# Performance work log

Measured on AMD Instinct MI355X. Metric: run time of the kernel, lower is better.

The kernel has to match this reference:

```python
import jax, jax.numpy as jnp
import numpy as np

T, B, D, H, DH = 2048, 2, 1024, 16, 64


def _rel_shift(x):
    # x: (Q, R, B, H) -- standard Transformer-XL relative shift via pad/reshape
    Q, R = x.shape[0], x.shape[1]
    zero_pad = jnp.zeros((Q, 1) + x.shape[2:], dtype=x.dtype)
    xp = jnp.concatenate([zero_pad, x], axis=1)          # (Q, R+1, B, H)
    xp = xp.reshape((R + 1, Q) + x.shape[2:])            # (R+1, Q, B, H)
    return xp[1:].reshape(x.shape)                       # (Q, R, B, H)


def setup_inputs() -> dict:
    key = jax.random.key(0)
    ks = jax.random.split(key, 7)
    w = jax.random.normal(ks[0], (T, B, D), dtype=jnp.float32)
    r = jax.random.normal(ks[1], (T, D), dtype=jnp.float32)
    w_qkv = jax.random.normal(ks[2], (3 * H * DH, D), dtype=jnp.float32) * 0.02
    w_r = jax.random.normal(ks[3], (H * DH, D), dtype=jnp.float32) * 0.02
    w_o = jax.random.normal(ks[4], (D, H * DH), dtype=jnp.float32) * 0.02
    r_r_bias = jax.random.normal(ks[5], (H, DH), dtype=jnp.float32) * 0.02
    attn_mask = jax.random.uniform(ks[6], (T, B)) < 0.1
    return {"w": w, "r": r, "w_qkv": w_qkv, "w_r": w_r, "w_o": w_o,
            "r_r_bias": r_r_bias, "attn_mask": attn_mask}


def reference(w, r, w_qkv, w_r, w_o, r_r_bias, attn_mask):
    qlen, bsz, d_model = w.shape
    n_head, d_head = r_r_bias.shape
    rlen = r.shape[0]
    scale = 1.0 / d_head ** 0.5

    heads = jnp.einsum('tbd,ed->tbe', w, w_qkv)           # (T, B, 3*H*DH)
    q, k, v = jnp.split(heads, 3, axis=-1)
    q = q.reshape(qlen, bsz, n_head, d_head)
    k = k.reshape(qlen, bsz, n_head, d_head)
    v = v.reshape(qlen, bsz, n_head, d_head)
    r_head_k = jnp.einsum('rd,ed->re', r, w_r).reshape(rlen, n_head, d_head)

    # NOTE: source uses r_r_bias for BOTH content and position biases
    rq = q + r_r_bias[None, None]                         # (Q, B, H, DH)
    AC = jnp.einsum('qbhd,kbhd->bhqk', rq, k)             # content scores
    BD = jnp.einsum('qbhd,rhd->bhqr', rq, r_head_k)       # position scores

    BD = jnp.transpose(BD, (2, 3, 0, 1))                  # (Q, R, B, H)
    BD = _rel_shift(BD)
    BD = jnp.transpose(BD, (2, 3, 0, 1))                  # (B, H, Q, R)
    BD = BD[:, :, :, :qlen]                               # klen == qlen

    score = (AC + BD) * scale                             # (B, H, Q, K)
    # key-padding mask (K, B) -> broadcast (B, 1, 1, K)
    score = jnp.where(attn_mask.T[:, None, None, :], -jnp.inf, score)

    prob = jax.nn.softmax(score.astype(jnp.float32), axis=-1).astype(score.dtype)
    attn_vec = jnp.einsum('bhqk,kbhd->qbhd', prob, v).reshape(qlen, bsz, n_head * d_head)
    out = jnp.einsum('qbe,de->qbd', attn_vec, w_o)        # (Q, B, D)
    return out, prob
```

## Files before the change

kernel.cpp:

```cpp
#include <hip/hip_runtime.h>
#include <hip/hip_bf16.h>
#include <cstdint>
#include <cstddef>

#define TLEN 2048
#define NB 2
#define DMODEL 1024
#define NH 16
#define NDH 64

typedef unsigned short ushortT;
typedef short bf16x8 __attribute__((ext_vector_type(8)));
typedef float f32x16 __attribute__((ext_vector_type(16)));

__device__ __forceinline__ ushortT f2bf(float f) {
  union { float f; unsigned int u; } x{f};
  unsigned int r = x.u + 0x7fff + ((x.u >> 16) & 1);
  return (ushortT)(r >> 16);
}
__device__ __forceinline__ unsigned int pk2(float lo, float hi) {
  return ((unsigned int)f2bf(hi) << 16) | (unsigned int)f2bf(lo);
}
__device__ __forceinline__ float bf2f(ushortT u) {
  union { unsigned int u; float f; } x;
  x.u = ((unsigned int)u) << 16;
  return x.f;
}

__device__ __forceinline__ void gld_lds16(const void* g, void* l) {
  __builtin_amdgcn_global_load_lds(
      (const __attribute__((address_space(1))) unsigned int*)g,
      (__attribute__((address_space(3))) unsigned int*)l, 16, 0, 0);
}


__global__ __launch_bounds__(256) void cvt_bf16(const float* __restrict__ in,
                                                ushortT* __restrict__ out, int n4) {
  int i = blockIdx.x * 256 + threadIdx.x;
  if (i < n4) {
    float4 v = reinterpret_cast<const float4*>(in)[i];
    ushort4 o;
    o.x = f2bf(v.x); o.y = f2bf(v.y); o.z = f2bf(v.z); o.w = f2bf(v.w);
    reinterpret_cast<ushort4*>(out)[i] = o;
  }
}

__global__ __launch_bounds__(256) void cvt_mask(const int* __restrict__ mask,
                                                float* __restrict__ mfl) {
  int j = blockIdx.x * 256 + threadIdx.x;
  if (j < TLEN) {
    mfl[j]        = mask[j * NB]     ? 0.f : 1.f;
    mfl[TLEN + j] = mask[j * NB + 1] ? 0.f : 1.f;
  }
}


template <typename Epi>
__global__ __launch_bounds__(256) void gemm_bf16(const ushortT* __restrict__ A,
                                                 const ushortT* __restrict__ B,
                                                 int K, Epi epi) {
  __shared__ ushortT Al[128 * 64];
  __shared__ ushortT Bl[128 * 64];
  const int tid = threadIdx.x;
  const int lane = tid & 63;
  const int wv = tid >> 6;
  const int wm = wv >> 1, wn = wv & 1;
  const int m0 = blockIdx.y * 128;
  const int n0 = blockIdx.x * 128;
  const int r32 = lane & 31;
  const int hh = lane >> 5;

  f32x16 acc[2][2];
#pragma unroll
  for (int i = 0; i < 2; ++i)
#pragma unroll
    for (int j = 0; j < 2; ++j)
#pragma unroll
      for (int e = 0; e < 16; ++e) acc[i][j][e] = 0.f;

  for (int k0 = 0; k0 < K; k0 += 64) {
#pragma unroll
    for (int it = 0; it < 4; ++it) {
      int idx = it * 256 + tid;
      int r = idx >> 3, c = idx & 7;
      int gcol = k0 + ((c ^ (r & 7)) << 3);
      gld_lds16(A + (size_t)(m0 + r) * K + gcol, Al + idx * 8);
      gld_lds16(B + (size_t)(n0 + r) * K + gcol, Bl + idx * 8);
    }
    asm volatile("s_waitcnt vmcnt(0)");
    __syncthreads();
#pragma unroll
    for (int kc = 0; kc < 4; ++kc) {
      int lc = kc * 2 + hh;
      bf16x8 af[2], bfr[2];
#pragma unroll
      for (int f = 0; f < 2; ++f) {
        int ar = wm * 64 + f * 32 + r32;
        af[f] = *(const bf16x8*)(Al + ar * 64 + ((lc ^ (ar & 7)) << 3));
        int br = wn * 64 + f * 32 + r32;
        bfr[f] = *(const bf16x8*)(Bl + br * 64 + ((lc ^ (br & 7)) << 3));
      }
#pragma unroll
      for (int i = 0; i < 2; ++i)
#pragma unroll
        for (int j = 0; j < 2; ++j)
          acc[i][j] = __builtin_amdgcn_mfma_f32_32x32x16_bf16(af[i], bfr[j],
                                                              acc[i][j], 0, 0, 0);
    }
    __syncthreads();
  }

#pragma unroll
  for (int i = 0; i < 2; ++i)
#pragma unroll
    for (int j = 0; j < 2; ++j)
#pragma unroll
      for (int rg = 0; rg < 16; ++rg) {
        int m = m0 + wm * 64 + i * 32 + (rg & 3) + 8 * (rg >> 2) + 4 * hh;
        int n = n0 + wn * 64 + j * 32 + r32;
        epi.store(m, n, acc[i][j][rg]);
      }
}

struct EpiQKV {
  ushortT* qb; ushortT* kb; ushortT* vtb; const float* bias;
  __device__ void store(int m, int n, float val) const {
    int t = m >> 1, b = m & 1;
    int which = n >> 10;
    int h = (n >> 6) & (NH - 1);
    int dh = n & (NDH - 1);
    int bh = b * NH + h;
    if (which == 0)
      qb[((size_t)bh * TLEN + t) * NDH + dh] = f2bf(val + bias[(h << 6) | dh]);
    else if (which == 1)
      kb[((size_t)bh * TLEN + t) * NDH + dh] = f2bf(val);
    else
      vtb[((size_t)bh * NDH + dh) * TLEN + t] = f2bf(val);
  }
};

struct EpiRK {
  ushortT* rk;
  __device__ void store(int m, int n, float val) const {
    int h = n >> 6, dh = n & 63;
    rk[((size_t)h * TLEN + m) * NDH + dh] = f2bf(val);
  }
};

struct EpiOut {
  float* out;
  __device__ void store(int m, int n, float val) const {
    out[(size_t)m * DMODEL + n] = val;
  }
};


__global__ __launch_bounds__(256) void attn_fast(
    const ushortT* __restrict__ qb, const ushortT* __restrict__ kb,
    const ushortT* __restrict__ vtb, const ushortT* __restrict__ rkb,
    const float* __restrict__ mfl, unsigned int* __restrict__ S,
    float* __restrict__ linv_g, ushortT* __restrict__ av_bf) {
  __shared__ float W[4][64][32];
  __shared__ float sl[4][32];

  const int bh = blockIdx.y;
  const int b = bh >> 4, h = bh & 15;
  const int wv = threadIdx.x >> 6;
  const int lane = threadIdx.x & 63;
  const int ql = lane & 31;
  const int hh = lane >> 5;
  const int qtile = wv & 1;
  const int jh = wv >> 1;
  const int q0 = blockIdx.x * 64 + qtile * 32;
  const int qg = q0 + ql;

  const ushortT* Qbh = qb + (size_t)bh * TLEN * NDH;
  const ushortT* Kbh = kb + (size_t)bh * TLEN * NDH;
  const ushortT* Vbh = vtb + (size_t)bh * NDH * TLEN;
  const ushortT* Rh  = rkb + (size_t)h * TLEN * NDH;
  const float* mflb  = mfl + (size_t)b * TLEN;
  unsigned int* Sb   = S + (size_t)bh * (TLEN / 2) * TLEN;
  float (*Wp)[32] = W[wv];

  bf16x8 Qf[4], Qs[4];
  {
    int r2 = min(qg + 1, TLEN - 1);
#pragma unroll
    for (int c = 0; c < 4; ++c) {
      Qf[c] = *(const bf16x8*)(Qbh + (size_t)qg * NDH + c * 16 + hh * 8);
      Qs[c] = *(const bf16x8*)(Qbh + (size_t)r2 * NDH + c * 16 + hh * 8);
    }
  }

  f32x16 pacc0, pacc1;
#pragma unroll
  for (int i = 0; i < 16; ++i) { pacc0[i] = 0.f; pacc1[i] = 0.f; }
  float l_acc = 0.f;

  const int jbeg = jh * (TLEN / 2);
  const int jend = jbeg + (TLEN / 2);
  for (int j0 = jbeg; j0 < jend; j0 += 32) {
    const int w1b = 2016 - q0 + j0;
    const int w2b = j0 - q0 - 33;
    const int base0 = (j0 <= q0) ? w1b : w2b;
    const int base1 = ((j0 < q0) ? w1b : w2b) + 32;
    const bool t0w1 = (j0 <= q0);
    const bool t1w1 = (j0 < q0);

    int r0 = max(0, min(base0 + ql, TLEN - 1));
    int r1 = max(0, min(base1 + ql, TLEN - 1));
    const ushortT* s0 = Rh + (size_t)r0 * NDH + hh * 8;
    const ushortT* s1 = Rh + (size_t)r1 * NDH + hh * 8;
    const ushortT* sk = Kbh + (size_t)(j0 + ql) * NDH + hh * 8;
    const ushortT* vrow0 = Vbh + (size_t)ql * TLEN + j0 + 8 * hh;
    const ushortT* vrow1 = Vbh + (size_t)(32 + ql) * TLEN + j0 + 8 * hh;
    bf16x8 rk0[4], rk1[4], kk[4];
#pragma unroll
    for (int c = 0; c < 4; ++c) {
      rk0[c] = *(const bf16x8*)(s0 + c * 16);
      rk1[c] = *(const bf16x8*)(s1 + c * 16);
      kk[c]  = *(const bf16x8*)(sk + c * 16);
    }
    bf16x8 v00 = *(const bf16x8*)(vrow0);
    bf16x8 v01 = *(const bf16x8*)(vrow0 + 16);
    bf16x8 v10 = *(const bf16x8*)(vrow1);
    bf16x8 v11 = *(const bf16x8*)(vrow1 + 16);
    float4 mf4[4];
#pragma unroll
    for (int g = 0; g < 4; ++g)
      mf4[g] = *(const float4*)(mflb + j0 + 8 * g + 4 * hh);

    f32x16 facc;
#pragma unroll
    for (int i = 0; i < 16; ++i) facc[i] = 0.f;
    __builtin_amdgcn_s_setprio(1);
#pragma unroll
    for (int c = 0; c < 4; ++c)
      facc = __builtin_amdgcn_mfma_f32_32x32x16_bf16(rk0[c], t0w1 ? Qf[c] : Qs[c], facc, 0, 0, 0);
    __builtin_amdgcn_s_setprio(0);
#pragma unroll
    for (int r = 0; r < 16; ++r)
      Wp[(r & 3) + 8 * (r >> 2) + 4 * hh][ql] = facc[r];

#pragma unroll
    for (int i = 0; i < 16; ++i) facc[i] = 0.f;
    __builtin_amdgcn_s_setprio(1);
#pragma unroll
    for (int c = 0; c < 4; ++c)
      facc = __builtin_amdgcn_mfma_f32_32x32x16_bf16(rk1[c], t1w1 ? Qf[c] : Qs[c], facc, 0, 0, 0);
    __builtin_amdgcn_s_setprio(0);
#pragma unroll
    for (int r = 0; r < 16; ++r)
      Wp[32 + (r & 3) + 8 * (r >> 2) + 4 * hh][ql] = facc[r];

    f32x16 cacc;
#pragma unroll
    for (int i = 0; i < 16; ++i) cacc[i] = 0.f;
    __builtin_amdgcn_s_setprio(1);
#pragma unroll
    for (int c = 0; c < 4; ++c)
      cacc = __builtin_amdgcn_mfma_f32_32x32x16_bf16(kk[c], Qf[c], cacc, 0, 0, 0);
    __builtin_amdgcn_s_setprio(0);

    float p[16];
#pragma unroll
    for (int r = 0; r < 16; ++r) {
      int jrow = (r & 3) + 8 * (r >> 2) + 4 * hh;
      int jg = j0 + jrow;
      float bd = (jg == qg + 1) ? 0.f : Wp[jrow - ql + 31][ql];
      float sc = (cacc[r] + bd) * 0.125f;
      float mv = (&mf4[r >> 2].x)[r & 3];
      float pv = mv * __expf(sc);
      p[r] = pv;
      l_acc += pv;
    }

    unsigned int u[8];
#pragma unroll
    for (int i = 0; i < 8; ++i) u[i] = pk2(p[2 * i], p[2 * i + 1]);

#pragma unroll
    for (int i = 0; i < 8; ++i) {
      int r = 2 * i;
      int jrow = (r & 3) + 8 * (r >> 2) + 4 * hh;
      Sb[(size_t)((j0 + jrow) >> 1) * TLEN + qg] = u[i];
    }

#pragma unroll
    for (int kh = 0; kh < 2; ++kh) {
      unsigned int t0 = (unsigned int)__shfl_xor((int)u[4 * kh + 0], 32);
      unsigned int t1 = (unsigned int)__shfl_xor((int)u[4 * kh + 1], 32);
      unsigned int t2 = (unsigned int)__shfl_xor((int)u[4 * kh + 2], 32);
      unsigned int t3 = (unsigned int)__shfl_xor((int)u[4 * kh + 3], 32);
      unsigned int fr[4];
      fr[0] = hh ? t2 : u[4 * kh + 0];
      fr[1] = hh ? t3 : u[4 * kh + 1];
      fr[2] = hh ? u[4 * kh + 2] : t0;
      fr[3] = hh ? u[4 * kh + 3] : t1;
      bf16x8 pa = *reinterpret_cast<bf16x8*>(fr);
      __builtin_amdgcn_s_setprio(1);
      pacc0 = __builtin_amdgcn_mfma_f32_32x32x16_bf16(pa, kh ? v01 : v00, pacc0, 0, 0, 0);
      pacc1 = __builtin_amdgcn_mfma_f32_32x32x16_bf16(pa, kh ? v11 : v10, pacc1, 0, 0, 0);
      __builtin_amdgcn_s_setprio(0);
    }
  }

#pragma unroll
  for (int r = 0; r < 16; ++r) {
    int qrow = (r & 3) + 8 * (r >> 2) + 4 * hh;
    Wp[qrow][ql] = pacc0[r];
    Wp[32 + qrow][ql] = pacc1[r];
  }
  float lh = l_acc + __shfl_xor(l_acc, 32);
  if (lane < 32) sl[wv][ql] = lh;
  __syncthreads();

  if (wv < 2) {
    if (lane < 32) {
      float lt = sl[wv][ql] + sl[wv + 2][ql];
      linv_g[(size_t)bh * TLEN + q0 + ql] = 1.0f / lt;
    }
#pragma unroll
    for (int r = 0; r < 16; ++r) {
      int qrow = (r & 3) + 8 * (r >> 2) + 4 * hh;
      float lt = sl[wv][qrow] + sl[wv + 2][qrow];
      float iv = 1.0f / lt;
      float s0v = W[wv][qrow][ql] + W[wv + 2][qrow][ql];
      float s1v = W[wv][32 + qrow][ql] + W[wv + 2][32 + qrow][ql];
      size_t aoff = ((size_t)(q0 + qrow) * NB + b) * DMODEL + h * NDH;
      av_bf[aoff + ql] = f2bf(s0v * iv);
      av_bf[aoff + 32 + ql] = f2bf(s1v * iv);
    }
  }
}


__global__ __launch_bounds__(256) void rescale_t(const unsigned int* __restrict__ S,
                                                 const float* __restrict__ linv_g,
                                                 float* __restrict__ prob) {
  __shared__ unsigned int lds[64][65];
  __shared__ float liv[64];
  const int qt = blockIdx.x;
  const int jt = blockIdx.y;
  const int bh = blockIdx.z;
  const int t = threadIdx.x;

  const unsigned int* Sb = S + ((size_t)bh * (TLEN / 2) + jt * 64) * TLEN + qt * 64;
  {
    int row = t >> 2, c0 = (t & 3) * 16;
#pragma unroll
    for (int k = 0; k < 4; ++k) {
      uint4 v = *reinterpret_cast<const uint4*>(Sb + (size_t)row * TLEN + c0 + k * 4);
      lds[row][c0 + k * 4 + 0] = v.x;
      lds[row][c0 + k * 4 + 1] = v.y;
      lds[row][c0 + k * 4 + 2] = v.z;
      lds[row][c0 + k * 4 + 3] = v.w;
    }
  }
  if (t < 64) liv[t] = linv_g[(size_t)bh * TLEN + qt * 64 + t];
  __syncthreads();

  float* P = prob + ((size_t)bh * TLEN + qt * 64) * TLEN + jt * 128;
#pragma unroll
  for (int k = 0; k < 8; ++k) {
    int idx = k * 256 + t;
    int row = idx >> 5, c4 = idx & 31;
    unsigned int u0 = lds[c4 * 2][row];
    unsigned int u1 = lds[c4 * 2 + 1][row];
    float iv = liv[row];
    float4 o;
    o.x = bf2f((ushortT)(u0 & 0xffff)) * iv;
    o.y = bf2f((ushortT)(u0 >> 16)) * iv;
    o.z = bf2f((ushortT)(u1 & 0xffff)) * iv;
    o.w = bf2f((ushortT)(u1 >> 16)) * iv;
    *reinterpret_cast<float4*>(P + (size_t)row * TLEN + c4 * 4) = o;
  }
}


__global__ __launch_bounds__(256) void attn_fused(
    const ushortT* __restrict__ qb, const ushortT* __restrict__ kb,
    const ushortT* __restrict__ vtb, const ushortT* __restrict__ rkb,
    const float* __restrict__ mfl, float* __restrict__ prob,
    ushortT* __restrict__ av_bf) {
  __shared__ float W[4][64][32];
  __shared__ float sl[4][32];
  __shared__ float linv[64];

  const int bh = blockIdx.y;
  const int b = bh >> 4, h = bh & 15;
  const int wv = threadIdx.x >> 6;
  const int lane = threadIdx.x & 63;
  const int ql = lane & 31;
  const int hh = lane >> 5;
  const int qtile = wv & 1;
  const int jh = wv >> 1;
  const int q0 = blockIdx.x * 64 + qtile * 32;
  const int qg = q0 + ql;

  const ushortT* Qbh = qb + (size_t)bh * TLEN * NDH;
  const ushortT* Kbh = kb + (size_t)bh * TLEN * NDH;
  const ushortT* Vbh = vtb + (size_t)bh * NDH * TLEN;
  const ushortT* Rh  = rkb + (size_t)h * TLEN * NDH;
  const float* mflb  = mfl + (size_t)b * TLEN;
  float (*Wp)[32] = W[wv];

  bf16x8 Qf[4], Qs[4];
  {
    int r2 = min(qg + 1, TLEN - 1);
#pragma unroll
    for (int c = 0; c < 4; ++c) {
      Qf[c] = *(const bf16x8*)(Qbh + (size_t)qg * NDH + c * 16 + hh * 8);
      Qs[c] = *(const bf16x8*)(Qbh + (size_t)r2 * NDH + c * 16 + hh * 8);
    }
  }

  f32x16 pacc0, pacc1;
#pragma unroll
  for (int i = 0; i < 16; ++i) { pacc0[i] = 0.f; pacc1[i] = 0.f; }
  float l_acc = 0.f;

  ushortT* pbrow = (ushortT*)prob + ((size_t)bh * TLEN + qg) * 4096 + 2048;

  const int jbeg = jh * (TLEN / 2);
  const int jend = jbeg + (TLEN / 2);
  for (int j0 = jbeg; j0 < jend; j0 += 32) {
    const int w1b = 2016 - q0 + j0;
    const int w2b = j0 - q0 - 33;
    const int base0 = (j0 <= q0) ? w1b : w2b;
    const int base1 = ((j0 < q0) ? w1b : w2b) + 32;
    const bool t0w1 = (j0 <= q0);
    const bool t1w1 = (j0 < q0);

    int r0 = max(0, min(base0 + ql, TLEN - 1));
    int r1 = max(0, min(base1 + ql, TLEN - 1));
    const ushortT* s0 = Rh + (size_t)r0 * NDH + hh * 8;
    const ushortT* s1 = Rh + (size_t)r1 * NDH + hh * 8;
    const ushortT* sk = Kbh + (size_t)(j0 + ql) * NDH + hh * 8;
    const ushortT* vrow0 = Vbh + (size_t)ql * TLEN + j0 + 8 * hh;
    const ushortT* vrow1 = Vbh + (size_t)(32 + ql) * TLEN + j0 + 8 * hh;
    bf16x8 rk0[4], rk1[4], kk[4];
#pragma unroll
    for (int c = 0; c < 4; ++c) {
      rk0[c] = *(const bf16x8*)(s0 + c * 16);
      rk1[c] = *(const bf16x8*)(s1 + c * 16);
      kk[c]  = *(const bf16x8*)(sk + c * 16);
    }
    bf16x8 v00 = *(const bf16x8*)(vrow0);
    bf16x8 v01 = *(const bf16x8*)(vrow0 + 16);
    bf16x8 v10 = *(const bf16x8*)(vrow1);
    bf16x8 v11 = *(const bf16x8*)(vrow1 + 16);
    float4 mf4[4];
#pragma unroll
    for (int g = 0; g < 4; ++g)
      mf4[g] = *(const float4*)(mflb + j0 + 8 * g + 4 * hh);

    f32x16 facc;
#pragma unroll
    for (int i = 0; i < 16; ++i) facc[i] = 0.f;
    __builtin_amdgcn_s_setprio(1);
#pragma unroll
    for (int c = 0; c < 4; ++c)
      facc = __builtin_amdgcn_mfma_f32_32x32x16_bf16(rk0[c], t0w1 ? Qf[c] : Qs[c], facc, 0, 0, 0);
    __builtin_amdgcn_s_setprio(0);
#pragma unroll
    for (int r = 0; r < 16; ++r)
      Wp[(r & 3) + 8 * (r >> 2) + 4 * hh][ql] = facc[r];

#pragma unroll
    for (int i = 0; i < 16; ++i) facc[i] = 0.f;
    __builtin_amdgcn_s_setprio(1);
#pragma unroll
    for (int c = 0; c < 4; ++c)
      facc = __builtin_amdgcn_mfma_f32_32x32x16_bf16(rk1[c], t1w1 ? Qf[c] : Qs[c], facc, 0, 0, 0);
    __builtin_amdgcn_s_setprio(0);
#pragma unroll
    for (int r = 0; r < 16; ++r)
      Wp[32 + (r & 3) + 8 * (r >> 2) + 4 * hh][ql] = facc[r];

    f32x16 cacc;
#pragma unroll
    for (int i = 0; i < 16; ++i) cacc[i] = 0.f;
    __builtin_amdgcn_s_setprio(1);
#pragma unroll
    for (int c = 0; c < 4; ++c)
      cacc = __builtin_amdgcn_mfma_f32_32x32x16_bf16(kk[c], Qf[c], cacc, 0, 0, 0);
    __builtin_amdgcn_s_setprio(0);

    float p[16];
#pragma unroll
    for (int r = 0; r < 16; ++r) {
      int jrow = (r & 3) + 8 * (r >> 2) + 4 * hh;
      int jg = j0 + jrow;
      float bd = (jg == qg + 1) ? 0.f : Wp[jrow - ql + 31][ql];
      float sc = (cacc[r] + bd) * 0.125f;
      float mv = (&mf4[r >> 2].x)[r & 3];
      float pv = mv * __expf(sc);
      p[r] = pv;
      l_acc += pv;
    }

#pragma unroll
    for (int g = 0; g < 4; ++g) {
      uint2 st;
      st.x = pk2(p[4 * g + 0], p[4 * g + 1]);
      st.y = pk2(p[4 * g + 2], p[4 * g + 3]);
      *reinterpret_cast<uint2*>(pbrow + j0 + 8 * g + 4 * hh) = st;
    }

#pragma unroll
    for (int kh = 0; kh < 2; ++kh) {
      unsigned int u0 = pk2(p[8 * kh + 0], p[8 * kh + 1]);
      unsigned int u1 = pk2(p[8 * kh + 2], p[8 * kh + 3]);
      unsigned int u2 = pk2(p[8 * kh + 4], p[8 * kh + 5]);
      unsigned int u3 = pk2(p[8 * kh + 6], p[8 * kh + 7]);
      unsigned int t0 = (unsigned int)__shfl_xor((int)u0, 32);
      unsigned int t1 = (unsigned int)__shfl_xor((int)u1, 32);
      unsigned int t2 = (unsigned int)__shfl_xor((int)u2, 32);
      unsigned int t3 = (unsigned int)__shfl_xor((int)u3, 32);
      unsigned int fr[4];
      fr[0] = hh ? t2 : u0;
      fr[1] = hh ? t3 : u1;
      fr[2] = hh ? u2 : t0;
      fr[3] = hh ? u3 : t1;
      bf16x8 pa = *reinterpret_cast<bf16x8*>(fr);
      __builtin_amdgcn_s_setprio(1);
      pacc0 = __builtin_amdgcn_mfma_f32_32x32x16_bf16(pa, kh ? v01 : v00, pacc0, 0, 0, 0);
      pacc1 = __builtin_amdgcn_mfma_f32_32x32x16_bf16(pa, kh ? v11 : v10, pacc1, 0, 0, 0);
      __builtin_amdgcn_s_setprio(0);
    }
  }

#pragma unroll
  for (int r = 0; r < 16; ++r) {
    int qrow = (r & 3) + 8 * (r >> 2) + 4 * hh;
    Wp[qrow][ql] = pacc0[r];
    Wp[32 + qrow][ql] = pacc1[r];
  }
  float lh = l_acc + __shfl_xor(l_acc, 32);
  if (lane < 32) sl[wv][ql] = lh;
  __syncthreads();

  if (wv < 2) {
    if (lane < 32) {
      float lt = sl[wv][ql] + sl[wv + 2][ql];
      linv[wv * 32 + ql] = 1.0f / lt;
    }
#pragma unroll
    for (int r = 0; r < 16; ++r) {
      int qrow = (r & 3) + 8 * (r >> 2) + 4 * hh;
      float lt = sl[wv][qrow] + sl[wv + 2][qrow];
      float iv = 1.0f / lt;
      float s0v = W[wv][qrow][ql] + W[wv + 2][qrow][ql];
      float s1v = W[wv][32 + qrow][ql] + W[wv + 2][32 + qrow][ql];
      size_t aoff = ((size_t)(q0 + qrow) * NB + b) * DMODEL + h * NDH;
      av_bf[aoff + ql] = f2bf(s0v * iv);
      av_bf[aoff + 32 + ql] = f2bf(s1v * iv);
    }
  }
  __syncthreads();

  const ushortT* probus = (const ushortT*)prob;
  const int lr = lane >> 4;
  const int cg = lane & 15;
  for (int s = 0; s < 8; ++s) {
    const int rloc = qtile * 32 + s * 4 + lr;
    const int rowg = blockIdx.x * 64 + rloc;
    const size_t ub = ((size_t)bh * TLEN + rowg) * 4096 + 2048 + jh * 1024 + cg * 8;
    const size_t fb = ((size_t)bh * TLEN + rowg) * 2048 + jh * 1024 + cg * 8;
    uint4 a[8];
#pragma unroll
    for (int k = 0; k < 8; ++k)
      a[k] = *reinterpret_cast<const uint4*>(probus + ub + k * 128);
    const float iv = linv[rloc];
    __syncthreads();
#pragma unroll
    for (int k = 0; k < 8; ++k) {
      float4 o0, o1;
      o0.x = bf2f((ushortT)(a[k].x & 0xffff)) * iv;
      o0.y = bf2f((ushortT)(a[k].x >> 16)) * iv;
      o0.z = bf2f((ushortT)(a[k].y & 0xffff)) * iv;
      o0.w = bf2f((ushortT)(a[k].y >> 16)) * iv;
      o1.x = bf2f((ushortT)(a[k].z & 0xffff)) * iv;
      o1.y = bf2f((ushortT)(a[k].z >> 16)) * iv;
      o1.z = bf2f((ushortT)(a[k].w & 0xffff)) * iv;
      o1.w = bf2f((ushortT)(a[k].w >> 16)) * iv;
      *reinterpret_cast<float4*>(prob + fb + k * 128) = o0;
      *reinterpret_cast<float4*>(prob + fb + k * 128 + 4) = o1;
    }
  }
}


extern "C" void kernel_launch(void* const* d_in, const int* in_sizes, int n_in,
                              void* d_out, int out_size, void* d_ws, size_t ws_size,
                              hipStream_t stream) {
  const float* w      = (const float*)d_in[0];
  const float* r      = (const float*)d_in[1];
  const float* w_qkv  = (const float*)d_in[2];
  const float* w_r    = (const float*)d_in[3];
  const float* w_o    = (const float*)d_in[4];
  const float* bias   = (const float*)d_in[5];
  const int* mask     = (const int*)d_in[6];

  float* out  = (float*)d_out;
  float* prob = out + (size_t)TLEN * NB * DMODEL;

  const size_t SZ = (size_t)NB * NH * TLEN * NDH;
  ushortT* w_bf    = (ushortT*)d_ws;
  ushortT* wqkv_bf = w_bf + (size_t)4096 * 1024;
  ushortT* r_bf    = wqkv_bf + (size_t)3072 * 1024;
  ushortT* wr_bf   = r_bf + (size_t)2048 * 1024;
  ushortT* wo_bf   = wr_bf + (size_t)1024 * 1024;
  ushortT* q_bf    = wo_bf + (size_t)1024 * 1024;
  ushortT* k_bf    = q_bf + SZ;
  ushortT* vt_bf   = k_bf + SZ;
  ushortT* rk_bf   = vt_bf + SZ;
  ushortT* av_bf   = rk_bf + SZ / 2;
  float* mfl       = (float*)(av_bf + SZ);
  float* linv_g    = mfl + (size_t)NB * TLEN;
  unsigned int* S  = (unsigned int*)(linv_g + (size_t)NB * NH * TLEN);
  const size_t need = (size_t)((char*)(S + (size_t)NB * NH * (TLEN / 2) * TLEN) -
                               (char*)d_ws);
  const bool fast = ws_size >= need;

  cvt_bf16<<<4096, 256, 0, stream>>>(w, w_bf, 4096 * 1024 / 4);
  cvt_bf16<<<3072, 256, 0, stream>>>(w_qkv, wqkv_bf, 3072 * 1024 / 4);
  cvt_bf16<<<2048, 256, 0, stream>>>(r, r_bf, 2048 * 1024 / 4);
  cvt_bf16<<<1024, 256, 0, stream>>>(w_r, wr_bf, 1024 * 1024 / 4);
  cvt_bf16<<<1024, 256, 0, stream>>>(w_o, wo_bf, 1024 * 1024 / 4);
  cvt_mask<<<8, 256, 0, stream>>>(mask, mfl);

  EpiQKV e1{q_bf, k_bf, vt_bf, bias};
  gemm_bf16<EpiQKV><<<dim3(3072 / 128, 4096 / 128), 256, 0, stream>>>(w_bf, wqkv_bf, DMODEL, e1);
  EpiRK e2{rk_bf};
  gemm_bf16<EpiRK><<<dim3(1024 / 128, 2048 / 128), 256, 0, stream>>>(r_bf, wr_bf, DMODEL, e2);

  if (fast) {
    attn_fast<<<dim3(32, 32), 256, 0, stream>>>(q_bf, k_bf, vt_bf, rk_bf,
                                                mfl, S, linv_g, av_bf);
    rescale_t<<<dim3(32, 16, 32), 256, 0, stream>>>(S, linv_g, prob);
  } else {
    attn_fused<<<dim3(32, 32), 256, 0, stream>>>(q_bf, k_bf, vt_bf, rk_bf,
                                                 mfl, prob, av_bf);
  }

  EpiOut e5{out};
  gemm_bf16<EpiOut><<<dim3(1024 / 128, 4096 / 128), 256, 0, stream>>>(av_bf, wo_bf, DMODEL, e5);
}
```

Before: 542.8 us.

## Stage K/V/R tiles in LDS and precompute extended rel-shifted R table

The position-key projection is written into an extended per-head table, with a zero row and a shifted duplicate, so the relative-shift indexing becomes one contiguous window with no clamping or diagonal special case. The fast attention kernel now uses 128 threads, each wave covering a 32-query tile over the full key range, and cooperatively loads swizzled K, V and R tiles into shared memory each step. This removes the cross-wave reduction at the end and the redundant per-wave global loads. The cost is a barrier per key step, lower block parallelism (two waves per block), and a larger R workspace written twice by the GEMM epilogue.

```diff
diff --git a/kernel.cpp b/kernel.cpp
--- a/kernel.cpp
+++ b/kernel.cpp
@@ -52,6 +52,13 @@
     mfl[j]        = mask[j * NB]     ? 0.f : 1.f;
     mfl[TLEN + j] = mask[j * NB + 1] ? 0.f : 1.f;
   }
+}
+
+__global__ __launch_bounds__(256) void zero_rkext(ushortT* __restrict__ rkE) {
+  int i = threadIdx.x;
+  int h = i >> 4, c = i & 15;
+  ushort4 z; z.x = 0; z.y = 0; z.z = 0; z.w = 0;
+  *reinterpret_cast<ushort4*>(rkE + ((size_t)h * 4096 + 2048) * NDH + c * 4) = z;
 }
 
 
@@ -140,10 +147,13 @@
 };
 
 struct EpiRK {
-  ushortT* rk;
+  ushortT* rkE;
   __device__ void store(int m, int n, float val) const {
     int h = n >> 6, dh = n & 63;
-    rk[((size_t)h * TLEN + m) * NDH + dh] = f2bf(val);
+    ushortT v = f2bf(val);
+    rkE[((size_t)h * 4096 + m) * NDH + dh] = v;
+    if (m <= 2046)
+      rkE[((size_t)h * 4096 + m + 2049) * NDH + dh] = v;
   }
 };
 
@@ -155,32 +165,33 @@
 };
 
 
-__global__ __launch_bounds__(256) void attn_fast(
+__global__ __launch_bounds__(128) void attn_fast(
     const ushortT* __restrict__ qb, const ushortT* __restrict__ kb,
-    const ushortT* __restrict__ vtb, const ushortT* __restrict__ rkb,
+    const ushortT* __restrict__ vtb, const ushortT* __restrict__ rkE,
     const float* __restrict__ mfl, unsigned int* __restrict__ S,
     float* __restrict__ linv_g, ushortT* __restrict__ av_bf) {
-  __shared__ float W[4][64][32];
-  __shared__ float sl[4][32];
+  __shared__ float W[2][64][32];
+  __shared__ ushortT KT[2048];
+  __shared__ ushortT VT[2048];
+  __shared__ ushortT RK[6144];
 
   const int bh = blockIdx.y;
   const int b = bh >> 4, h = bh & 15;
-  const int wv = threadIdx.x >> 6;
+  const int t = threadIdx.x >> 6;
   const int lane = threadIdx.x & 63;
   const int ql = lane & 31;
   const int hh = lane >> 5;
-  const int qtile = wv & 1;
-  const int jh = wv >> 1;
-  const int q0 = blockIdx.x * 64 + qtile * 32;
+  const int Q0 = blockIdx.x * 64;
+  const int q0 = Q0 + 32 * t;
   const int qg = q0 + ql;
 
   const ushortT* Qbh = qb + (size_t)bh * TLEN * NDH;
   const ushortT* Kbh = kb + (size_t)bh * TLEN * NDH;
   const ushortT* Vbh = vtb + (size_t)bh * NDH * TLEN;
-  const ushortT* Rh  = rkb + (size_t)h * TLEN * NDH;
+  const ushortT* Rh  = rkE + (size_t)h * 4096 * NDH;
   const float* mflb  = mfl + (size_t)b * TLEN;
   unsigned int* Sb   = S + (size_t)bh * (TLEN / 2) * TLEN;
-  float (*Wp)[32] = W[wv];
+  float (*Wp)[32] = W[t];
 
   bf16x8 Qf[4], Qs[4];
   {
@@ -197,46 +208,44 @@
   for (int i = 0; i < 16; ++i) { pacc0[i] = 0.f; pacc1[i] = 0.f; }
   float l_acc = 0.f;
 
-  const int jbeg = jh * (TLEN / 2);
-  const int jend = jbeg + (TLEN / 2);
-  for (int j0 = jbeg; j0 < jend; j0 += 32) {
-    const int w1b = 2016 - q0 + j0;
-    const int w2b = j0 - q0 - 33;
-    const int base0 = (j0 <= q0) ? w1b : w2b;
-    const int base1 = ((j0 < q0) ? w1b : w2b) + 32;
+  for (int j0 = 0; j0 < TLEN; j0 += 32) {
+    __syncthreads();
+    const int U = 1984 + j0 - Q0;
+#pragma unroll
+    for (int i = 0; i < 6; ++i) {
+      int ci = (t * 6 + i) * 64 + lane;
+      int row = ci >> 3, c = ci & 7;
+      gld_lds16(Rh + (size_t)(U + row) * NDH + ((c ^ (row & 7)) << 3), RK + ci * 8);
+    }
+#pragma unroll
+    for (int i = 0; i < 2; ++i) {
+      int ci = (t * 2 + i) * 64 + lane;
+      int row = ci >> 3, c = ci & 7;
+      gld_lds16(Kbh + (size_t)(j0 + row) * NDH + ((c ^ (row & 7)) << 3), KT + ci * 8);
+      int d = ci >> 2, c2 = ci & 3;
+      gld_lds16(Vbh + (size_t)d * TLEN + j0 + ((c2 ^ (d & 3)) << 3), VT + ci * 8);
+    }
+    float4 mf4[4];
+#pragma unroll
+    for (int g = 0; g < 4; ++g)
+      mf4[g] = *(const float4*)(mflb + j0 + 8 * g + 4 * hh);
+    asm volatile("s_waitcnt vmcnt(0)");
+    __syncthreads();
+
     const bool t0w1 = (j0 <= q0);
     const bool t1w1 = (j0 < q0);
-
-    int r0 = max(0, min(base0 + ql, TLEN - 1));
-    int r1 = max(0, min(base1 + ql, TLEN - 1));
-    const ushortT* s0 = Rh + (size_t)r0 * NDH + hh * 8;
-    const ushortT* s1 = Rh + (size_t)r1 * NDH + hh * 8;
-    const ushortT* sk = Kbh + (size_t)(j0 + ql) * NDH + hh * 8;
-    const ushortT* vrow0 = Vbh + (size_t)ql * TLEN + j0 + 8 * hh;
-    const ushortT* vrow1 = Vbh + (size_t)(32 + ql) * TLEN + j0 + 8 * hh;
-    bf16x8 rk0[4], rk1[4], kk[4];
-#pragma unroll
-    for (int c = 0; c < 4; ++c) {
-      rk0[c] = *(const bf16x8*)(s0 + c * 16);
-      rk1[c] = *(const bf16x8*)(s1 + c * 16);
-      kk[c]  = *(const bf16x8*)(sk + c * 16);
-    }
-    bf16x8 v00 = *(const bf16x8*)(vrow0);
-    bf16x8 v01 = *(const bf16x8*)(vrow0 + 16);
-    bf16x8 v10 = *(const bf16x8*)(vrow1);
-    bf16x8 v11 = *(const bf16x8*)(vrow1 + 16);
-    float4 mf4[4];
-#pragma unroll
-    for (int g = 0; g < 4; ++g)
-      mf4[g] = *(const float4*)(mflb + j0 + 8 * g + 4 * hh);
+    const int R1 = 32 * (1 - t) + ql;
+    const int R2 = R1 + 32;
 
     f32x16 facc;
 #pragma unroll
     for (int i = 0; i < 16; ++i) facc[i] = 0.f;
     __builtin_amdgcn_s_setprio(1);
 #pragma unroll
-    for (int c = 0; c < 4; ++c)
-      facc = __builtin_amdgcn_mfma_f32_32x32x16_bf16(rk0[c], t0w1 ? Qf[c] : Qs[c], facc, 0, 0, 0);
+    for (int c = 0; c < 4; ++c) {
+      bf16x8 a = *(const bf16x8*)(RK + R1 * NDH + (((2 * c + hh) ^ (R1 & 7)) << 3));
+      facc = __builtin_amdgcn_mfma_f32_32x32x16_bf16(a, t0w1 ? Qf[c] : Qs[c], facc, 0, 0, 0);
+    }
     __builtin_amdgcn_s_setprio(0);
 #pragma unroll
     for (int r = 0; r < 16; ++r)
@@ -246,8 +255,10 @@
     for (int i = 0; i < 16; ++i) facc[i] = 0.f;
     __builtin_amdgcn_s_setprio(1);
 #pragma unroll
-    for (int c = 0; c < 4; ++c)
-      facc = __builtin_amdgcn_mfma_f32_32x32x16_bf16(rk1[c], t1w1 ? Qf[c] : Qs[c], facc, 0, 0, 0);
+    for (int c = 0; c < 4; ++c) {
+      bf16x8 a = *(const bf16x8*)(RK + R2 * NDH + (((2 * c + hh) ^ (R2 & 7)) << 3));
+      facc = __builtin_amdgcn_mfma_f32_32x32x16_bf16(a, t1w1 ? Qf[c] : Qs[c], facc, 0, 0, 0);
+    }
     __builtin_amdgcn_s_setprio(0);
 #pragma unroll
     for (int r = 0; r < 16; ++r)
@@ -258,16 +269,17 @@
     for (int i = 0; i < 16; ++i) cacc[i] = 0.f;
     __builtin_amdgcn_s_setprio(1);
 #pragma unroll
-    for (int c = 0; c < 4; ++c)
-      cacc = __builtin_amdgcn_mfma_f32_32x32x16_bf16(kk[c], Qf[c], cacc, 0, 0, 0);
+    for (int c = 0; c < 4; ++c) {
+      bf16x8 a = *(const bf16x8*)(KT + ql * NDH + (((2 * c + hh) ^ (ql & 7)) << 3));
+      cacc = __builtin_amdgcn_mfma_f32_32x32x16_bf16(a, Qf[c], cacc, 0, 0, 0);
+    }
     __builtin_amdgcn_s_setprio(0);
 
     float p[16];
 #pragma unroll
     for (int r = 0; r < 16; ++r) {
       int jrow = (r & 3) + 8 * (r >> 2) + 4 * hh;
-      int jg = j0 + jrow;
-      float bd = (jg == qg + 1) ? 0.f : Wp[jrow - ql + 31][ql];
+      float bd = Wp[jrow - ql + 31][ql];
       float sc = (cacc[r] + bd) * 0.125f;
       float mv = (&mf4[r >> 2].x)[r & 3];
       float pv = mv * __expf(sc);
@@ -298,39 +310,25 @@
       fr[2] = hh ? u[4 * kh + 2] : t0;
       fr[3] = hh ? u[4 * kh + 3] : t1;
       bf16x8 pa = *reinterpret_cast<bf16x8*>(fr);
+      bf16x8 v0 = *(const bf16x8*)(VT + ql * 32 + (((2 * kh + hh) ^ (ql & 3)) << 3));
+      bf16x8 v1 = *(const bf16x8*)(VT + (32 + ql) * 32 + (((2 * kh + hh) ^ (ql & 3)) << 3));
       __builtin_amdgcn_s_setprio(1);
-      pacc0 = __builtin_amdgcn_mfma_f32_32x32x16_bf16(pa, kh ? v01 : v00, pacc0, 0, 0, 0);
-      pacc1 = __builtin_amdgcn_mfma_f32_32x32x16_bf16(pa, kh ? v11 : v10, pacc1, 0, 0, 0);
+      pacc0 = __builtin_amdgcn_mfma_f32_32x32x16_bf16(pa, v0, pacc0, 0, 0, 0);
+      pacc1 = __builtin_amdgcn_mfma_f32_32x32x16_bf16(pa, v1, pacc1, 0, 0, 0);
       __builtin_amdgcn_s_setprio(0);
     }
   }
 
+  float lt = l_acc + __shfl_xor(l_acc, 32);
+  if (lane < 32) linv_g[(size_t)bh * TLEN + qg] = 1.0f / lt;
+  float inv = 1.0f / lt;
 #pragma unroll
   for (int r = 0; r < 16; ++r) {
     int qrow = (r & 3) + 8 * (r >> 2) + 4 * hh;
-    Wp[qrow][ql] = pacc0[r];
-    Wp[32 + qrow][ql] = pacc1[r];
-  }
-  float lh = l_acc + __shfl_xor(l_acc, 32);
-  if (lane < 32) sl[wv][ql] = lh;
-  __syncthreads();
-
-  if (wv < 2) {
-    if (lane < 32) {
-      float lt = sl[wv][ql] + sl[wv + 2][ql];
-      linv_g[(size_t)bh * TLEN + q0 + ql] = 1.0f / lt;
-    }
-#pragma unroll
-    for (int r = 0; r < 16; ++r) {
-      int qrow = (r & 3) + 8 * (r >> 2) + 4 * hh;
-      float lt = sl[wv][qrow] + sl[wv + 2][qrow];
-      float iv = 1.0f / lt;
-      float s0v = W[wv][qrow][ql] + W[wv + 2][qrow][ql];
-      float s1v = W[wv][32 + qrow][ql] + W[wv + 2][32 + qrow][ql];
-      size_t aoff = ((size_t)(q0 + qrow) * NB + b) * DMODEL + h * NDH;
-      av_bf[aoff + ql] = f2bf(s0v * iv);
-      av_bf[aoff + 32 + ql] = f2bf(s1v * iv);
-    }
+    float iv = __shfl(inv, qrow);
+    size_t aoff = ((size_t)(q0 + qrow) * NB + b) * DMODEL + h * NDH;
+    av_bf[aoff + ql] = f2bf(pacc0[r] * iv);
+    av_bf[aoff + 32 + ql] = f2bf(pacc1[r] * iv);
   }
 }
 
@@ -380,7 +378,7 @@
 
 __global__ __launch_bounds__(256) void attn_fused(
     const ushortT* __restrict__ qb, const ushortT* __restrict__ kb,
-    const ushortT* __restrict__ vtb, const ushortT* __restrict__ rkb,
+    const ushortT* __restrict__ vtb, const ushortT* __restrict__ rkE,
     const float* __restrict__ mfl, float* __restrict__ prob,
     ushortT* __restrict__ av_bf) {
   __shared__ float W[4][64][32];
@@ -401,7 +399,7 @@
   const ushortT* Qbh = qb + (size_t)bh * TLEN * NDH;
   const ushortT* Kbh = kb + (size_t)bh * TLEN * NDH;
   const ushortT* Vbh = vtb + (size_t)bh * NDH * TLEN;
-  const ushortT* Rh  = rkb + (size_t)h * TLEN * NDH;
+  const ushortT* Rh  = rkE + (size_t)h * 4096 * NDH;
   const float* mflb  = mfl + (size_t)b * TLEN;
   float (*Wp)[32] = W[wv];
 
@@ -425,17 +423,12 @@
   const int jbeg = jh * (TLEN / 2);
   const int jend = jbeg + (TLEN / 2);
   for (int j0 = jbeg; j0 < jend; j0 += 32) {
-    const int w1b = 2016 - q0 + j0;
-    const int w2b = j0 - q0 - 33;
-    const int base0 = (j0 <= q0) ? w1b : w2b;
-    const int base1 = ((j0 < q0) ? w1b : w2b) + 32;
+    const int base_t = 2016 + j0 - q0;
     const bool t0w1 = (j0 <= q0);
     const bool t1w1 = (j0 < q0);
 
-    int r0 = max(0, min(base0 + ql, TLEN - 1));
-    int r1 = max(0, min(base1 + ql, TLEN - 1));
-    const ushortT* s0 = Rh + (size_t)r0 * NDH + hh * 8;
-    const ushortT* s1 = Rh + (size_t)r1 * NDH + hh * 8;
+    const ushortT* s0 = Rh + (size_t)(base_t + ql) * NDH + hh * 8;
+    const ushortT* s1 = Rh + (size_t)(base_t + 32 + ql) * NDH + hh * 8;
     const ushortT* sk = Kbh + (size_t)(j0 + ql) * NDH + hh * 8;
     const ushortT* vrow0 = Vbh + (size_t)ql * TLEN + j0 + 8 * hh;
     const ushortT* vrow1 = Vbh + (size_t)(32 + ql) * TLEN + j0 + 8 * hh;
@@ -491,8 +484,7 @@
 #pragma unroll
     for (int r = 0; r < 16; ++r) {
       int jrow = (r & 3) + 8 * (r >> 2) + 4 * hh;
-      int jg = j0 + jrow;
-      float bd = (jg == qg + 1) ? 0.f : Wp[jrow - ql + 31][ql];
+      float bd = Wp[jrow - ql + 31][ql];
       float sc = (cacc[r] + bd) * 0.125f;
       float mv = (&mf4[r >> 2].x)[r & 3];
       float pv = mv * __expf(sc);
@@ -615,8 +607,8 @@
   ushortT* q_bf    = wo_bf + (size_t)1024 * 1024;
   ushortT* k_bf    = q_bf + SZ;
   ushortT* vt_bf   = k_bf + SZ;
-  ushortT* rk_bf   = vt_bf + SZ;
-  ushortT* av_bf   = rk_bf + SZ / 2;
+  ushortT* rkE_bf  = vt_bf + SZ;
+  ushortT* av_bf   = rkE_bf + (size_t)NH * 4096 * NDH;
   float* mfl       = (float*)(av_bf + SZ);
   float* linv_g    = mfl + (size_t)NB * TLEN;
   unsigned int* S  = (unsigned int*)(linv_g + (size_t)NB * NH * TLEN);
@@ -630,18 +622,19 @@
   cvt_bf16<<<1024, 256, 0, stream>>>(w_r, wr_bf, 1024 * 1024 / 4);
   cvt_bf16<<<1024, 256, 0, stream>>>(w_o, wo_bf, 1024 * 1024 / 4);
   cvt_mask<<<8, 256, 0, stream>>>(mask, mfl);
+  zero_rkext<<<1, 256, 0, stream>>>(rkE_bf);
 
   EpiQKV e1{q_bf, k_bf, vt_bf, bias};
   gemm_bf16<EpiQKV><<<dim3(3072 / 128, 4096 / 128), 256, 0, stream>>>(w_bf, wqkv_bf, DMODEL, e1);
-  EpiRK e2{rk_bf};
+  EpiRK e2{rkE_bf};
   gemm_bf16<EpiRK><<<dim3(1024 / 128, 2048 / 128), 256, 0, stream>>>(r_bf, wr_bf, DMODEL, e2);
 
   if (fast) {
-    attn_fast<<<dim3(32, 32), 256, 0, stream>>>(q_bf, k_bf, vt_bf, rk_bf,
+    attn_fast<<<dim3(32, 32), 128, 0, stream>>>(q_bf, k_bf, vt_bf, rkE_bf,
                                                 mfl, S, linv_g, av_bf);
     rescale_t<<<dim3(32, 16, 32), 256, 0, stream>>>(S, linv_g, prob);
   } else {
-    attn_fused<<<dim3(32, 32), 256, 0, stream>>>(q_bf, k_bf, vt_bf, rk_bf,
+    attn_fused<<<dim3(32, 32), 256, 0, stream>>>(q_bf, k_bf, vt_bf, rkE_bf,
                                                  mfl, prob, av_bf);
   }
 
```

Result: faster. 471.3 us (-13.2%).
